# Kernel optimization log

Hardware: AMD Instinct MI355X
Metric: run time of the kernel (lower is better)

The kernel has to match this reference:

```python
import jax, jax.numpy as jnp
import numpy as np

H_SIZE = 2048
NUM_K_HEADS = 16
NUM_V_HEADS = 32
DK = 128
DV = 128
KEY_DIM = NUM_K_HEADS * DK        # 2048
VALUE_DIM = NUM_V_HEADS * DV      # 4096
CONV_DIM = 2 * KEY_DIM + VALUE_DIM  # 8192
KERNEL = 4
EPS = 1e-6
B, S = 2, 2048


def setup_inputs() -> dict:
    key = jax.random.key(0)
    ks = jax.random.split(key, 8)
    w = lambda k, shape, s: jax.random.normal(k, shape, jnp.float32) * s
    return {
        "hidden_states": jax.random.normal(ks[0], (B, S, H_SIZE), jnp.float32),
        "w_qkv": w(ks[1], (H_SIZE, CONV_DIM), 0.02),
        "w_z": w(ks[2], (H_SIZE, VALUE_DIM), 0.02),
        "w_b": w(ks[3], (H_SIZE, NUM_V_HEADS), 0.02),
        "w_a": w(ks[4], (H_SIZE, NUM_V_HEADS), 0.02),
        "conv_w": w(ks[5], (CONV_DIM, KERNEL), 0.2),
        "dt_bias": jnp.ones((NUM_V_HEADS,), jnp.float32),
        "A_log": jnp.zeros((NUM_V_HEADS,), jnp.float32),
        "norm_gamma": jnp.ones((DV,), jnp.float32),
        "w_out": w(ks[6], (VALUE_DIM, H_SIZE), 0.02),
    }


def _l2norm(x, eps=1e-6):
    return x * jax.lax.rsqrt(jnp.sum(x * x, axis=-1, keepdims=True) + eps)


def _causal_conv(x, w):
    # depthwise causal conv1d; x: (B,S,C), w: (C,K)
    K = w.shape[-1]
    Sq = x.shape[1]
    xp = jnp.pad(x, ((0, 0), (K - 1, 0), (0, 0)))
    out = xp[:, 0:Sq, :] * w[None, None, :, 0]
    for j in range(1, K):  # tiny fixed kernel loop (K=4)
        out = out + xp[:, j:j + Sq, :] * w[None, None, :, j]
    return out


def _forward(hidden_states, w_qkv, w_z, w_b, w_a, conv_w, dt_bias, A_log,
             norm_gamma, w_out):
    Bq, Sq, _ = hidden_states.shape
    mixed = hidden_states @ w_qkv                       # (B,S,CONV_DIM)
    z = (hidden_states @ w_z).reshape(Bq, Sq, NUM_V_HEADS, DV)
    b = hidden_states @ w_b                             # (B,S,Hv)
    a = hidden_states @ w_a                             # (B,S,Hv)
    mixed = jax.nn.silu(_causal_conv(mixed, conv_w))
    q, k, v = jnp.split(mixed, [KEY_DIM, 2 * KEY_DIM], axis=-1)
    q = q.reshape(Bq, Sq, NUM_K_HEADS, DK)
    k = k.reshape(Bq, Sq, NUM_K_HEADS, DK)
    v = v.reshape(Bq, Sq, NUM_V_HEADS, DV)
    nrep = NUM_V_HEADS // NUM_K_HEADS
    q = jnp.repeat(q, nrep, axis=2)                     # GQA expand -> Hv heads
    k = jnp.repeat(k, nrep, axis=2)
    beta = jax.nn.sigmoid(b)                            # write gate
    g = -jnp.exp(A_log)[None, None, :] * jax.nn.softplus(a + dt_bias[None, None, :])

    # gated delta rule recurrence in float32 (matches reference)
    qf = _l2norm(q.astype(jnp.float32)) * (DK ** -0.5)
    kf = _l2norm(k.astype(jnp.float32))
    vf = v.astype(jnp.float32)
    gf = g.astype(jnp.float32)
    bf = beta.astype(jnp.float32)

    def step(state, xs):
        q_t, k_t, v_t, g_t, b_t = xs  # (B,H,dk),(B,H,dk),(B,H,dv),(B,H),(B,H)
        state = state * jnp.exp(g_t)[..., None, None]
        kv = jnp.einsum('bhk,bhkv->bhv', k_t, state)
        delta = (v_t - kv) * b_t[..., None]
        state = state + jnp.einsum('bhk,bhv->bhkv', k_t, delta)
        out = jnp.einsum('bhk,bhkv->bhv', q_t, state)
        return state, out

    mv = lambda x: jnp.moveaxis(x, 1, 0)  # (B,S,...) -> (S,B,...)
    xs = (mv(qf), mv(kf), mv(vf), mv(gf), mv(bf))
    state0 = jnp.zeros((Bq, NUM_V_HEADS, DK, DV), jnp.float32)
    _, outs = jax.lax.scan(step, state0, xs)            # (S,B,H,dv)
    o = jnp.moveaxis(outs, 0, 1)                        # (B,S,H,dv)

    # gated RMSNorm over head_v_dim: gate with silu(z), then rms-normalize
    o = o * jax.nn.silu(z.astype(jnp.float32))
    o = o * jax.lax.rsqrt(jnp.mean(o * o, axis=-1, keepdims=True) + EPS)
    o = o * norm_gamma
    o = o.reshape(Bq, Sq, VALUE_DIM).astype(hidden_states.dtype)
    return o @ w_out


def reference(hidden_states, w_qkv, w_z, w_b, w_a, conv_w, dt_bias, A_log,
              norm_gamma, w_out):
    return _forward(hidden_states, w_qkv, w_z, w_b, w_a, conv_w, dt_bias,
                    A_log, norm_gamma, w_out)
```

## Files before the change

### kernel.cpp

```cpp
#include <hip/hip_runtime.h>
#include <hip/hip_bf16.h>
#include <cstdint>


#define HSZ 2048
#define NUM_K_HEADS 16
#define NUM_V_HEADS 32
#define DKH 128
#define DVH 128
#define KEY_DIM 2048
#define VALUE_DIM 4096
#define CONV_DIM 8192
#define BB 2
#define SSEQ 2048
#define MM (BB * SSEQ)
#define CHUNK 64
#define NCHUNK (SSEQ / CHUNK)
#define DVB 16

typedef __hip_bfloat16 bf16;
typedef short short8 __attribute__((ext_vector_type(8)));
typedef float f32x4 __attribute__((ext_vector_type(4)));

__device__ __forceinline__ float bfu(ushort u) {
  union { float f; uint32_t i; } x;
  x.i = ((uint32_t)u) << 16;
  return x.f;
}
__device__ __forceinline__ ushort f2b(float f) {
  bf16 h = __float2bfloat16(f);
  return *reinterpret_cast<ushort*>(&h);
}

__device__ __forceinline__ void gload16(const void* g, const void* l) {
  __builtin_amdgcn_global_load_lds(
      (const __attribute__((address_space(1))) unsigned int*)g,
      (__attribute__((address_space(3))) unsigned int*)(const_cast<void*>(l)),
      16, 0, 0);
}

__device__ __forceinline__ int kidx(int r, int d) {
  return r * 128 + (((d >> 3) ^ (r & 7)) << 3) + (d & 7);
}
__device__ __forceinline__ int widx(int r, int d) {
  return r * 64 + (((d >> 3) ^ (r & 7)) << 3) + (d & 7);
}

__global__ __launch_bounds__(256) void cast_bf16_kernel(
    const float* __restrict__ in, ushort* __restrict__ out, int n4) {
  int i = blockIdx.x * 256 + threadIdx.x;
  if (i < n4) {
    float4 v = ((const float4*)in)[i];
    ushort4 u;
    u.x = f2b(v.x); u.y = f2b(v.y); u.z = f2b(v.z); u.w = f2b(v.w);
    ((ushort4*)out)[i] = u;
  }
}

__global__ __launch_bounds__(256) void transpose_cast(
    const float* __restrict__ W, ushort* __restrict__ WT, int K, int N) {
  __shared__ ushort tile[32][33];
  const int tx = threadIdx.x & 31, ty = threadIdx.x >> 5;
  const int n0 = blockIdx.x * 32, k0 = blockIdx.y * 32;
#pragma unroll
  for (int i = 0; i < 4; ++i)
    tile[ty + i * 8][tx] = f2b(W[(size_t)(k0 + ty + i * 8) * N + n0 + tx]);
  __syncthreads();
#pragma unroll
  for (int i = 0; i < 4; ++i)
    WT[(size_t)(n0 + ty + i * 8) * K + k0 + tx] = tile[tx][ty + i * 8];
}

__global__ __launch_bounds__(512) void gemm256(
    const ushort* __restrict__ A, const ushort* __restrict__ BT,
    ushort* __restrict__ Cv, int M, int N, int K) {
  __shared__ __align__(16) ushort smem[256 * 264];
  const int t = threadIdx.x;
  const int w = t >> 6, lane = t & 63;
  const int m0 = blockIdx.y * 256, n0 = blockIdx.x * 256;
  const int wm = (w >> 2) * 128, wn = (w & 3) * 64;
  const int fr = lane & 15, kb = lane >> 4;
  const int srow = t >> 3;
  const int scol = (t & 7) * 8;
  const int ssw = ((scol >> 3) ^ (srow & 7)) << 3;
  const int rsw = fr & 7;
  f32x4 acc[8][4] = {};
  const int nt = K / 64;

#define STAGE_TILE(tt, buf)                                                   \
  {                                                                           \
    const int k0_ = (tt)*64;                                                  \
    ushort* As_ = smem + (buf)*32768;                                         \
    ushort* Bs_ = As_ + 16384;                                                \
    _Pragma("unroll") for (int p = 0; p < 4; ++p) {                           \
      const int row_ = p * 64 + srow;                                         \
      gload16(&A[(size_t)(m0 + row_) * K + k0_ + ssw],                        \
              &As_[row_ * 64 + scol]);                                        \
    }                                                                         \
    _Pragma("unroll") for (int p = 0; p < 4; ++p) {                           \
      const int row_ = p * 64 + srow;                                         \
      gload16(&BT[(size_t)(n0 + row_) * K + k0_ + ssw],                       \
              &Bs_[row_ * 64 + scol]);                                        \
    }                                                                         \
  }

  STAGE_TILE(0, 0);
  STAGE_TILE(1, 1);

  for (int tt = 0; tt < nt; ++tt) {
    const int buf = tt & 1;
    const ushort* As = smem + buf * 32768;
    const ushort* Bs = As + 16384;
    if (tt + 1 < nt)
      asm volatile("s_waitcnt vmcnt(8)" ::: "memory");
    else
      asm volatile("s_waitcnt vmcnt(0)" ::: "memory");
    __builtin_amdgcn_sched_barrier(0);
    __builtin_amdgcn_s_barrier();
    __builtin_amdgcn_sched_barrier(0);
#pragma unroll
    for (int ks = 0; ks < 2; ++ks) {
      const int kg = ks * 4 + kb;
      const int ca = ((kg ^ rsw) << 3);
      short8 af[8], bf_[4];
#pragma unroll
      for (int mf = 0; mf < 8; ++mf)
        af[mf] = *(const short8*)&As[(wm + mf * 16 + fr) * 64 + ca];
#pragma unroll
      for (int nf = 0; nf < 4; ++nf)
        bf_[nf] = *(const short8*)&Bs[(wn + nf * 16 + fr) * 64 + ca];
#pragma unroll
      for (int mf = 0; mf < 8; ++mf)
#pragma unroll
        for (int nf = 0; nf < 4; ++nf)
          acc[mf][nf] = __builtin_amdgcn_mfma_f32_16x16x32_bf16(
              af[mf], bf_[nf], acc[mf][nf], 0, 0, 0);
    }
    __builtin_amdgcn_sched_barrier(0);
    __builtin_amdgcn_s_barrier();
    __builtin_amdgcn_sched_barrier(0);
    if (tt + 2 < nt) STAGE_TILE(tt + 2, buf);
  }
#undef STAGE_TILE

  const int crow = wm + (lane >> 4) * 4;
  const int ccol = wn + fr;
#pragma unroll
  for (int mf = 0; mf < 8; ++mf)
#pragma unroll
    for (int nf = 0; nf < 4; ++nf)
#pragma unroll
      for (int j = 0; j < 4; ++j)
        smem[(crow + mf * 16 + j) * 264 + ccol + nf * 16] = f2b(acc[mf][nf][j]);
  __syncthreads();
#pragma unroll
  for (int p = 0; p < 16; ++p) {
    const int r = p * 16 + (t >> 5), cch = (t & 31) * 8;
    *(short8*)&Cv[(size_t)(m0 + r) * N + n0 + cch] =
        *(const short8*)&smem[r * 264 + cch];
  }
}

__global__ __launch_bounds__(256) void gemm_mfma_f32(
    const ushort* __restrict__ A, const ushort* __restrict__ BT,
    float* __restrict__ C, int M, int N, int K) {
  __shared__ ushort As[128 * 64];
  __shared__ ushort Bs[128 * 64];
  const int t = threadIdx.x;
  const int w = t >> 6, lane = t & 63;
  const int m0 = blockIdx.y * 128, n0 = blockIdx.x * 128;
  const int srow = lane >> 3;
  const int scol = (lane & 7) * 8;
  const int wm = (w >> 1) * 64, wn = (w & 1) * 64;
  const int fr = lane & 15, kb = lane >> 4;
  f32x4 acc[4][4] = {};

  for (int k0 = 0; k0 < K; k0 += 64) {
#pragma unroll
    for (int i = 0; i < 4; ++i) {
      const int row = (i * 4 + w) * 8 + srow;
      gload16(&A[(size_t)(m0 + row) * K + k0 + scol], &As[row * 64 + scol]);
      gload16(&BT[(size_t)(n0 + row) * K + k0 + scol], &Bs[row * 64 + scol]);
    }
    __syncthreads();
#pragma unroll
    for (int ks = 0; ks < 2; ++ks) {
      const int ka = ks * 32 + kb * 8;
      short8 af[4], bfr[4];
#pragma unroll
      for (int mf = 0; mf < 4; ++mf)
        af[mf] = *(const short8*)&As[(wm + mf * 16 + fr) * 64 + ka];
#pragma unroll
      for (int nf = 0; nf < 4; ++nf)
        bfr[nf] = *(const short8*)&Bs[(wn + nf * 16 + fr) * 64 + ka];
#pragma unroll
      for (int mf = 0; mf < 4; ++mf)
#pragma unroll
        for (int nf = 0; nf < 4; ++nf)
          acc[mf][nf] = __builtin_amdgcn_mfma_f32_16x16x32_bf16(
              af[mf], bfr[nf], acc[mf][nf], 0, 0, 0);
    }
    __syncthreads();
  }
  const int orow = m0 + wm + (lane >> 4) * 4;
  const int ocol = n0 + wn + fr;
#pragma unroll
  for (int mf = 0; mf < 4; ++mf)
#pragma unroll
    for (int nf = 0; nf < 4; ++nf)
#pragma unroll
      for (int j = 0; j < 4; ++j)
        C[(size_t)(orow + mf * 16 + j) * N + ocol + nf * 16] = acc[mf][nf][j];
}

__global__ __launch_bounds__(256) void ba_kernel(
    const float* __restrict__ hs, const float* __restrict__ w_b,
    const float* __restrict__ w_a, const float* __restrict__ dt_bias,
    const float* __restrict__ A_log, float* __restrict__ gbuf,
    float* __restrict__ beta) {
  const int row0 = blockIdx.x * 8;
  const int t = threadIdx.x;
  __shared__ float hsr[8][HSZ];
  __shared__ float red[2][256];
  {
    const float4* src = (const float4*)(hs + (size_t)row0 * HSZ);
    for (int i = t; i < 8 * HSZ / 4; i += 256) ((float4*)hsr)[i] = src[i];
  }
  __syncthreads();
  const int h = t & 31, p = t >> 5;
  float sb[8] = {}, sa[8] = {};
  const int kbeg = p * 256;
  for (int k = kbeg; k < kbeg + 256; ++k) {
    float wb = w_b[k * NUM_V_HEADS + h];
    float wa = w_a[k * NUM_V_HEADS + h];
#pragma unroll
    for (int r = 0; r < 8; ++r) {
      float x = hsr[r][k];
      sb[r] += x * wb;
      sa[r] += x * wa;
    }
  }
#pragma unroll
  for (int r = 0; r < 8; ++r) {
    red[0][t] = sb[r];
    red[1][t] = sa[r];
    __syncthreads();
    if (t < NUM_V_HEADS) {
      float b = 0.f, a = 0.f;
#pragma unroll
      for (int q = 0; q < 8; ++q) {
        b += red[0][t + 32 * q];
        a += red[1][t + 32 * q];
      }
      float bet = 1.f / (1.f + expf(-b));
      float x = a + dt_bias[t];
      float sp = (x > 20.f) ? x : log1pf(expf(x));
      gbuf[(size_t)(row0 + r) * NUM_V_HEADS + t] = -expf(A_log[t]) * sp;
      beta[(size_t)(row0 + r) * NUM_V_HEADS + t] = bet;
    }
    __syncthreads();
  }
}

__global__ __launch_bounds__(256) void conv_kernel(
    const ushort* __restrict__ mixed, const float* __restrict__ conv_w,
    ushort* __restrict__ qkv) {
  const int bid = blockIdx.x;
  const int slice = bid & 3;
  const int row0 = (bid >> 2) * 8;
  const int s0 = row0 & (SSEQ - 1);
  const int t = threadIdx.x;
  const int cbase = slice * 2048 + t * 8;

  float wreg[4][8];
#pragma unroll
  for (int e = 0; e < 8; ++e) {
    float4 wv = *(const float4*)&conv_w[(cbase + e) * 4];
    wreg[0][e] = wv.x;
    wreg[1][e] = wv.y;
    wreg[2][e] = wv.z;
    wreg[3][e] = wv.w;
  }

  const ushort* mp = mixed + (size_t)row0 * CONV_DIM + cbase;
  short8 win[4];
  const short8 z8 = {0, 0, 0, 0, 0, 0, 0, 0};
#pragma unroll
  for (int j = 0; j < 3; ++j)
    win[j] = (s0 - 3 + j >= 0) ? *(const short8*)&mp[(ptrdiff_t)(j - 3) * CONV_DIM]
                               : z8;

  if (slice < 2) {
    float vals[8][8];
    float ssq[8];
#pragma unroll
    for (int r = 0; r < 8; ++r) {
      win[3] = *(const short8*)&mp[(ptrdiff_t)r * CONV_DIM];
      float sq = 0.f;
#pragma unroll
      for (int e = 0; e < 8; ++e) {
        float a = bfu((ushort)win[0][e]) * wreg[0][e] +
                  bfu((ushort)win[1][e]) * wreg[1][e] +
                  bfu((ushort)win[2][e]) * wreg[2][e] +
                  bfu((ushort)win[3][e]) * wreg[3][e];
        float x = a / (1.f + expf(-a));
        vals[r][e] = x;
        sq += x * x;
      }
      ssq[r] = sq;
      win[0] = win[1];
      win[1] = win[2];
      win[2] = win[3];
    }
#pragma unroll
    for (int r = 0; r < 8; ++r) {
      float sq = ssq[r];
      sq += __shfl_xor(sq, 1, 64);
      sq += __shfl_xor(sq, 2, 64);
      sq += __shfl_xor(sq, 4, 64);
      sq += __shfl_xor(sq, 8, 64);
      float sc = rsqrtf(sq + 1e-6f);
      if (slice == 0) sc *= 0.08838834764831845f;
      short8 o;
#pragma unroll
      for (int e = 0; e < 8; ++e) o[e] = (short)f2b(vals[r][e] * sc);
      *(short8*)&qkv[(size_t)(row0 + r) * CONV_DIM + cbase] = o;
    }
  } else {
#pragma unroll
    for (int r = 0; r < 8; ++r) {
      win[3] = *(const short8*)&mp[(ptrdiff_t)r * CONV_DIM];
      short8 o;
#pragma unroll
      for (int e = 0; e < 8; ++e) {
        float a = bfu((ushort)win[0][e]) * wreg[0][e] +
                  bfu((ushort)win[1][e]) * wreg[1][e] +
                  bfu((ushort)win[2][e]) * wreg[2][e] +
                  bfu((ushort)win[3][e]) * wreg[3][e];
        o[e] = (short)f2b(a / (1.f + expf(-a)));
      }
      *(short8*)&qkv[(size_t)(row0 + r) * CONV_DIM + cbase] = o;
      win[0] = win[1];
      win[1] = win[2];
      win[2] = win[3];
    }
  }
}

__global__ __launch_bounds__(256) void chunk_T_kernel(
    const ushort* __restrict__ qkv, const float* __restrict__ gbuf,
    const float* __restrict__ beta, ushort* __restrict__ Tbuf,
    ushort* __restrict__ Wbuf) {
  const int bid = blockIdx.x;
  const int c = bid & 31;
  const int h = (bid >> 5) & 31;
  const int b = bid >> 10;
  const int hk = h >> 1;
  const int t = threadIdx.x;
  const int w = t >> 6, lane = t & 63;
  const int fr = lane & 15, fq = lane >> 4;

  __shared__ ushort Klds[64 * 128];
  __shared__ ushort Qlds[64 * 128];
  __shared__ __align__(16) float AT[64][68];
  __shared__ ushort Wlds[64 * 64];
  __shared__ float Gs[64], Bsh[64];

  const int row0 = b * SSEQ + c * CHUNK;
  const int qcol = hk * DKH;
  const int kcol = KEY_DIM + hk * DKH;

#pragma unroll
  for (int r = 0; r < 4; ++r) {
    int vi = t + 256 * r;
    int row = vi >> 4, gr = vi & 15;
    const size_t gb = (size_t)(row0 + row) * CONV_DIM;
    *(short8*)&Klds[row * 128 + ((gr ^ (row & 7)) << 3)] =
        *(const short8*)&qkv[gb + kcol + gr * 8];
    *(short8*)&Qlds[row * 128 + ((gr ^ (row & 7)) << 3)] =
        *(const short8*)&qkv[gb + qcol + gr * 8];
  }
  if (t < 64) {
    float s = gbuf[(size_t)(row0 + t) * NUM_V_HEADS + h];
#pragma unroll
    for (int off = 1; off < 64; off <<= 1) {
      float p = __shfl_up(s, off, 64);
      if (lane >= off) s += p;
    }
    Gs[t] = s;
    Bsh[t] = beta[(size_t)(row0 + t) * NUM_V_HEADS + h];
  }
  __syncthreads();

  f32x4 kkt[4] = {}, qkt[4] = {};
#pragma unroll
  for (int ks = 0; ks < 4; ++ks) {
    int d0 = ks * 32 + fq * 8;
    short8 xk = *(const short8*)&Klds[kidx(w * 16 + fr, d0)];
    short8 xq = *(const short8*)&Qlds[kidx(w * 16 + fr, d0)];
#pragma unroll
    for (int j = 0; j < 4; ++j) {
      short8 yk = *(const short8*)&Klds[kidx(j * 16 + fr, d0)];
      kkt[j] = __builtin_amdgcn_mfma_f32_16x16x32_bf16(xk, yk, kkt[j], 0, 0, 0);
      qkt[j] = __builtin_amdgcn_mfma_f32_16x16x32_bf16(xq, yk, qkt[j], 0, 0, 0);
    }
  }
#pragma unroll
  for (int j = 0; j < 4; ++j)
#pragma unroll
    for (int jj = 0; jj < 4; ++jj) {
      int i = w * 16 + fq * 4 + jj;
      int jc = j * 16 + fr;
      AT[jc][i] = (jc < i) ? Bsh[i] * __expf(Gs[i] - Gs[jc]) * kkt[j][jj] : 0.f;
      float val = (jc <= i) ? __expf(Gs[i] - Gs[jc]) * qkt[j][jj] : 0.f;
      Wlds[widx(i, jc)] = f2b(val);
    }
  __syncthreads();

  {
    ushort* Wg = Wbuf + (size_t)bid * 4096;
#pragma unroll
    for (int e = 0; e < 8; ++e)
      ((uint*)Wg)[e * 256 + t] = ((const uint*)Wlds)[e * 256 + t];
  }

  if (w == 0) {
    float u[64];
#pragma unroll
    for (int i = 0; i < 64; ++i) u[i] = (i == lane) ? 1.f : 0.f;
#pragma unroll
    for (int j = 0; j < 63; ++j) {
      float xj = u[j];
      const int i0 = (j + 1) & ~3;
#pragma unroll
      for (int ii = i0; ii < 64; ii += 4) {
        float4 a4 = *(const float4*)&AT[j][ii];
        if (ii + 0 > j) u[ii + 0] -= a4.x * xj;
        if (ii + 1 > j) u[ii + 1] -= a4.y * xj;
        if (ii + 2 > j) u[ii + 2] -= a4.z * xj;
        if (ii + 3 > j) u[ii + 3] -= a4.w * xj;
      }
    }
    ushort* Tg = Tbuf + (size_t)bid * 4096;
#pragma unroll
    for (int i = 0; i < 64; ++i) Tg[i * 64 + lane] = f2b(u[i]);
  }
}

__global__ __launch_bounds__(256, 2) void recur_chunk_kernel(
    const ushort* __restrict__ qkv, const float* __restrict__ gbuf,
    const float* __restrict__ beta, const ushort* __restrict__ Tbuf,
    const ushort* __restrict__ Wbuf, float* __restrict__ o) {
  const int bid = blockIdx.x;
  const int dvq = bid & 7;
  const int h = (bid >> 3) & 31;
  const int b = bid >> 8;
  const int hk = h >> 1;
  const int t = threadIdx.x;
  const int w = t >> 6, lane = t & 63;
  const int fr = lane & 15, fq = lane >> 4;

  __shared__ ushort Klds[64 * 128];
  __shared__ ushort Vlds[64 * DVB];
  __shared__ ushort Sth[DVB * 128];
  __shared__ ushort Stl[DVB * 128];
  __shared__ ushort Th[64 * 64];
  __shared__ ushort Wlds[64 * 64];
  __shared__ ushort Ut[DVB * 64];
  __shared__ ushort UTs[DVB * 64];
  __shared__ ushort UTo[DVB * 64];
  __shared__ float Gs[64], Bsh[64];

  float sreg[2][4] = {};

  const int qcol = hk * DKH;
  const int kcol = KEY_DIM + hk * DKH;
  const int vcol = 2 * KEY_DIM + h * DVH + dvq * DVB;
  const int ocol = h * DVH + dvq * DVB;
  const size_t tbase0 = ((size_t)(b * 32 + h) * 32) * 4096;

  for (int c = 0; c < NCHUNK; ++c) {
    const int row0 = b * SSEQ + c * CHUNK;

    short8 xq[4];
#pragma unroll
    for (int ks = 0; ks < 4; ++ks)
      xq[ks] = *(const short8*)&qkv[(size_t)(row0 + w * 16 + fr) * CONV_DIM +
                                    qcol + ks * 32 + fq * 8];
    const ushort* Tg = Tbuf + tbase0 + (size_t)c * 4096;
    const ushort* Wg = Wbuf + tbase0 + (size_t)c * 4096;
    short8 tv0 = *(const short8*)&Tg[t * 16];
    short8 tv1 = *(const short8*)&Tg[t * 16 + 8];
#pragma unroll
    for (int e = 0; e < 8; ++e)
      ((uint*)Wlds)[e * 256 + t] = ((const uint*)Wg)[e * 256 + t];
#pragma unroll
    for (int r = 0; r < 4; ++r) {
      int vi = t + 256 * r;
      int row = vi >> 4, gr = vi & 15;
      *(short8*)&Klds[row * 128 + ((gr ^ (row & 7)) << 3)] =
          *(const short8*)&qkv[(size_t)(row0 + row) * CONV_DIM + kcol + gr * 8];
    }
    if (t < 128) {
      int row = t >> 1, c0 = (t & 1) * 8;
      *(short8*)&Vlds[row * DVB + c0] =
          *(const short8*)&qkv[(size_t)(row0 + row) * CONV_DIM + vcol + c0];
    }
    if (t < 64) {
      float s = gbuf[(size_t)(row0 + t) * NUM_V_HEADS + h];
#pragma unroll
      for (int off = 1; off < 64; off <<= 1) {
        float p = __shfl_up(s, off, 64);
        if (lane >= off) s += p;
      }
      Gs[t] = s;
      Bsh[t] = beta[(size_t)(row0 + t) * NUM_V_HEADS + h];
    }
#pragma unroll
    for (int dt = 0; dt < 2; ++dt)
#pragma unroll
      for (int jj = 0; jj < 4; ++jj) {
        int d = (w * 2 + dt) * 16 + fq * 4 + jj;
        float f = sreg[dt][jj];
        ushort hi = f2b(f);
        int idx = kidx(fr, d);
        Sth[idx] = hi;
        Stl[idx] = f2b(f - bfu(hi));
      }
    {
      int r = t >> 2, d0 = (t & 3) * 16;
      *(short8*)&Th[widx(r, d0)] = tv0;
      *(short8*)&Th[widx(r, d0 + 8)] = tv1;
    }
    __syncthreads();

    f32x4 ks0 = {}, qs0 = {};
#pragma unroll
    for (int ks = 0; ks < 4; ++ks) {
      int d0 = ks * 32 + fq * 8;
      short8 xk = *(const short8*)&Klds[kidx(w * 16 + fr, d0)];
      short8 yh = *(const short8*)&Sth[kidx(fr, d0)];
      short8 yl = *(const short8*)&Stl[kidx(fr, d0)];
      ks0 = __builtin_amdgcn_mfma_f32_16x16x32_bf16(xk, yh, ks0, 0, 0, 0);
      ks0 = __builtin_amdgcn_mfma_f32_16x16x32_bf16(xk, yl, ks0, 0, 0, 0);
      qs0 = __builtin_amdgcn_mfma_f32_16x16x32_bf16(xq[ks], yh, qs0, 0, 0, 0);
      qs0 = __builtin_amdgcn_mfma_f32_16x16x32_bf16(xq[ks], yl, qs0, 0, 0, 0);
    }
    f32x4 oacc;
#pragma unroll
    for (int jj = 0; jj < 4; ++jj) {
      int i = w * 16 + fq * 4 + jj;
      float eg = __expf(Gs[i]);
      float rhs = Bsh[i] * (bfu(Vlds[i * DVB + fr]) - eg * ks0[jj]);
      Ut[widx(fr, i)] = f2b(rhs);
      oacc[jj] = qs0[jj] * eg;
    }
    __syncthreads();

    {
      f32x4 uacc = {};
#pragma unroll
      for (int ks = 0; ks < 2; ++ks) {
        int j0 = ks * 32 + fq * 8;
        short8 ta = *(const short8*)&Th[widx(w * 16 + fr, j0)];
        short8 ub = *(const short8*)&Ut[widx(fr, j0)];
        uacc = __builtin_amdgcn_mfma_f32_16x16x32_bf16(ta, ub, uacc, 0, 0, 0);
      }
#pragma unroll
      for (int jj = 0; jj < 4; ++jj) {
        int i = w * 16 + fq * 4 + jj;
        float u = uacc[jj];
        UTo[widx(fr, i)] = f2b(u);
        UTs[widx(fr, i)] = f2b(u * __expf(Gs[63] - Gs[i]));
      }
    }
    __syncthreads();

#pragma unroll
    for (int ks = 0; ks < 2; ++ks) {
      int i0 = ks * 32 + fq * 8;
      short8 xw = *(const short8*)&Wlds[widx(w * 16 + fr, i0)];
      short8 yu = *(const short8*)&UTo[widx(fr, i0)];
      oacc = __builtin_amdgcn_mfma_f32_16x16x32_bf16(xw, yu, oacc, 0, 0, 0);
    }
#pragma unroll
    for (int jj = 0; jj < 4; ++jj) {
      int tt = w * 16 + fq * 4 + jj;
      o[(size_t)(row0 + tt) * VALUE_DIM + ocol + fr] = oacc[jj];
    }
    {
      float eGC = __expf(Gs[63]);
#pragma unroll
      for (int dt = 0; dt < 2; ++dt) {
        const int dk0 = (w * 2 + dt) * 16;
        f32x4 sacc;
#pragma unroll
        for (int jj = 0; jj < 4; ++jj) sacc[jj] = sreg[dt][jj] * eGC;
        const int dkr = dk0 + fr;
#pragma unroll
        for (int ks = 0; ks < 2; ++ks) {
          short8 xk;
#pragma unroll
          for (int e = 0; e < 8; ++e)
            xk[e] = (short)Klds[kidx(ks * 32 + fq * 8 + e, dkr)];
          short8 yu = *(const short8*)&UTs[widx(fr, ks * 32 + fq * 8)];
          sacc = __builtin_amdgcn_mfma_f32_16x16x32_bf16(xk, yu, sacc, 0, 0, 0);
        }
#pragma unroll
        for (int jj = 0; jj < 4; ++jj) sreg[dt][jj] = sacc[jj];
      }
    }
    __syncthreads();
  }
}

__global__ __launch_bounds__(256) void gnorm_kernel(
    const float* __restrict__ o, const ushort* __restrict__ z,
    const float* __restrict__ gamma, ushort* __restrict__ ob) {
  const int row = blockIdx.x;
  const int t = threadIdx.x;
  const int grp = t >> 3, r = t & 7;
  const float* op = o + (size_t)row * VALUE_DIM + grp * DVH + r * 16;
  const ushort* zp = z + (size_t)row * VALUE_DIM + grp * DVH + r * 16;
  ushort* obp = ob + (size_t)row * VALUE_DIM + grp * DVH + r * 16;
  float vals[16];
  float ssq = 0.f;
#pragma unroll
  for (int i = 0; i < 16; ++i) {
    float zz = bfu(zp[i]);
    float x = op[i] * (zz / (1.f + expf(-zz)));
    vals[i] = x;
    ssq += x * x;
  }
  ssq += __shfl_xor(ssq, 1, 64);
  ssq += __shfl_xor(ssq, 2, 64);
  ssq += __shfl_xor(ssq, 4, 64);
  float sc = rsqrtf(ssq * (1.f / 128.f) + 1e-6f);
#pragma unroll
  for (int i = 0; i < 16; ++i) obp[i] = f2b(vals[i] * sc * gamma[r * 16 + i]);
}

extern "C" void kernel_launch(void* const* d_in, const int* in_sizes, int n_in,
                              void* d_out, int out_size, void* d_ws,
                              size_t ws_size, hipStream_t stream) {
  const float* hs = (const float*)d_in[0];
  const float* w_qkv = (const float*)d_in[1];
  const float* w_z = (const float*)d_in[2];
  const float* w_b = (const float*)d_in[3];
  const float* w_a = (const float*)d_in[4];
  const float* conv_w = (const float*)d_in[5];
  const float* dt_bias = (const float*)d_in[6];
  const float* A_log = (const float*)d_in[7];
  const float* gamma = (const float*)d_in[8];
  const float* w_out = (const float*)d_in[9];
  float* out = (float*)d_out;
  char* wsb = (char*)d_ws;

  ushort* hs_b = (ushort*)wsb;
  ushort* wqkvT = hs_b + (size_t)MM * HSZ;
  ushort* wzT = wqkvT + (size_t)CONV_DIM * HSZ;
  ushort* woutT = wzT + (size_t)VALUE_DIM * HSZ;
  ushort* mixed = woutT + (size_t)HSZ * VALUE_DIM;
  ushort* qkv = mixed + (size_t)MM * CONV_DIM;
  ushort* z = qkv + (size_t)MM * CONV_DIM;
  float* gbuf = (float*)(z + (size_t)MM * VALUE_DIM);
  float* beta = gbuf + (size_t)MM * NUM_V_HEADS;
  float* o = (float*)mixed;
  ushort* ob = qkv;
  ushort* Tbuf = hs_b;
  ushort* Wbuf = wqkvT;

  cast_bf16_kernel<<<(MM * HSZ / 4 + 255) / 256, 256, 0, stream>>>(
      hs, hs_b, MM * HSZ / 4);
  transpose_cast<<<dim3(CONV_DIM / 32, HSZ / 32), 256, 0, stream>>>(
      w_qkv, wqkvT, HSZ, CONV_DIM);
  transpose_cast<<<dim3(VALUE_DIM / 32, HSZ / 32), 256, 0, stream>>>(
      w_z, wzT, HSZ, VALUE_DIM);
  transpose_cast<<<dim3(HSZ / 32, VALUE_DIM / 32), 256, 0, stream>>>(
      w_out, woutT, VALUE_DIM, HSZ);

  gemm256<<<dim3(CONV_DIM / 256, MM / 256), 512, 0, stream>>>(
      hs_b, wqkvT, mixed, MM, CONV_DIM, HSZ);
  gemm256<<<dim3(VALUE_DIM / 256, MM / 256), 512, 0, stream>>>(
      hs_b, wzT, z, MM, VALUE_DIM, HSZ);
  ba_kernel<<<MM / 8, 256, 0, stream>>>(hs, w_b, w_a, dt_bias, A_log, gbuf,
                                        beta);
  conv_kernel<<<2048, 256, 0, stream>>>(mixed, conv_w, qkv);
  chunk_T_kernel<<<2048, 256, 0, stream>>>(qkv, gbuf, beta, Tbuf, Wbuf);
  recur_chunk_kernel<<<512, 256, 0, stream>>>(qkv, gbuf, beta, Tbuf, Wbuf, o);
  gnorm_kernel<<<MM, 256, 0, stream>>>(o, z, gamma, ob);
  gemm_mfma_f32<<<dim3(HSZ / 128, MM / 128), 256, 0, stream>>>(
      ob, woutT, out, MM, HSZ, VALUE_DIM);
}
```

Measured before the change: 729.6 us.

## Double-buffer output GEMM with swizzled LDS and vectorize gated norm

The output projection GEMM now double-buffers its LDS tiles, prefetching two k-steps ahead with explicit vmcnt waits and raw s_barrier calls so global loads overlap with MFMA work. It also applies an XOR swizzle to LDS columns to reduce bank conflicts, and sets launch bounds to allow two blocks per CU. Separately, the gated RMSNorm kernel now uses vectorized float4 and short8 loads and stores. The cost is doubled LDS use per block and more delicate synchronization that depends on exact vmcnt counting.

New measurement: 695.1 us. 1.05x faster.

```diff
diff --git a/kernel.cpp b/kernel.cpp
--- a/kernel.cpp
+++ b/kernel.cpp
@@ -161,38 +161,64 @@
   }
 }
 
-__global__ __launch_bounds__(256) void gemm_mfma_f32(
+__global__ __launch_bounds__(256, 2) void gemm128_f32(
     const ushort* __restrict__ A, const ushort* __restrict__ BT,
     float* __restrict__ C, int M, int N, int K) {
-  __shared__ ushort As[128 * 64];
-  __shared__ ushort Bs[128 * 64];
+  __shared__ __align__(16) ushort smem[2 * 16384];
   const int t = threadIdx.x;
   const int w = t >> 6, lane = t & 63;
   const int m0 = blockIdx.y * 128, n0 = blockIdx.x * 128;
-  const int srow = lane >> 3;
-  const int scol = (lane & 7) * 8;
   const int wm = (w >> 1) * 64, wn = (w & 1) * 64;
   const int fr = lane & 15, kb = lane >> 4;
+  const int srow = t >> 3;
+  const int scol = (t & 7) * 8;
+  const int ssw = ((scol >> 3) ^ (srow & 7)) << 3;
+  const int rsw = fr & 7;
   f32x4 acc[4][4] = {};
-
-  for (int k0 = 0; k0 < K; k0 += 64) {
-#pragma unroll
-    for (int i = 0; i < 4; ++i) {
-      const int row = (i * 4 + w) * 8 + srow;
-      gload16(&A[(size_t)(m0 + row) * K + k0 + scol], &As[row * 64 + scol]);
-      gload16(&BT[(size_t)(n0 + row) * K + k0 + scol], &Bs[row * 64 + scol]);
-    }
-    __syncthreads();
+  const int nt = K / 64;
+
+#define STAGE128(tt, buf)                                                     \
+  {                                                                           \
+    const int k0_ = (tt)*64;                                                  \
+    ushort* As_ = smem + (buf)*16384;                                         \
+    ushort* Bs_ = As_ + 8192;                                                 \
+    _Pragma("unroll") for (int p = 0; p < 4; ++p) {                           \
+      const int row_ = p * 32 + srow;                                         \
+      gload16(&A[(size_t)(m0 + row_) * K + k0_ + ssw],                        \
+              &As_[row_ * 64 + scol]);                                        \
+    }                                                                         \
+    _Pragma("unroll") for (int p = 0; p < 4; ++p) {                           \
+      const int row_ = p * 32 + srow;                                         \
+      gload16(&BT[(size_t)(n0 + row_) * K + k0_ + ssw],                       \
+              &Bs_[row_ * 64 + scol]);                                        \
+    }                                                                         \
+  }
+
+  STAGE128(0, 0);
+  STAGE128(1, 1);
+
+  for (int tt = 0; tt < nt; ++tt) {
+    const int buf = tt & 1;
+    const ushort* As = smem + buf * 16384;
+    const ushort* Bs = As + 8192;
+    if (tt + 1 < nt)
+      asm volatile("s_waitcnt vmcnt(8)" ::: "memory");
+    else
+      asm volatile("s_waitcnt vmcnt(0)" ::: "memory");
+    __builtin_amdgcn_sched_barrier(0);
+    __builtin_amdgcn_s_barrier();
+    __builtin_amdgcn_sched_barrier(0);
 #pragma unroll
     for (int ks = 0; ks < 2; ++ks) {
-      const int ka = ks * 32 + kb * 8;
+      const int kg = ks * 4 + kb;
+      const int ca = ((kg ^ rsw) << 3);
       short8 af[4], bfr[4];
 #pragma unroll
       for (int mf = 0; mf < 4; ++mf)
-        af[mf] = *(const short8*)&As[(wm + mf * 16 + fr) * 64 + ka];
+        af[mf] = *(const short8*)&As[(wm + mf * 16 + fr) * 64 + ca];
 #pragma unroll
       for (int nf = 0; nf < 4; ++nf)
-        bfr[nf] = *(const short8*)&Bs[(wn + nf * 16 + fr) * 64 + ka];
+        bfr[nf] = *(const short8*)&Bs[(wn + nf * 16 + fr) * 64 + ca];
 #pragma unroll
       for (int mf = 0; mf < 4; ++mf)
 #pragma unroll
@@ -200,8 +226,13 @@
           acc[mf][nf] = __builtin_amdgcn_mfma_f32_16x16x32_bf16(
               af[mf], bfr[nf], acc[mf][nf], 0, 0, 0);
     }
-    __syncthreads();
-  }
+    __builtin_amdgcn_sched_barrier(0);
+    __builtin_amdgcn_s_barrier();
+    __builtin_amdgcn_sched_barrier(0);
+    if (tt + 2 < nt) STAGE128(tt + 2, buf);
+  }
+#undef STAGE128
+
   const int orow = m0 + wm + (lane >> 4) * 4;
   const int ocol = n0 + wn + fr;
 #pragma unroll
@@ -623,12 +654,19 @@
   const float* op = o + (size_t)row * VALUE_DIM + grp * DVH + r * 16;
   const ushort* zp = z + (size_t)row * VALUE_DIM + grp * DVH + r * 16;
   ushort* obp = ob + (size_t)row * VALUE_DIM + grp * DVH + r * 16;
+  float4 ov[4];
+  short8 zv[2];
+#pragma unroll
+  for (int q = 0; q < 4; ++q) ov[q] = *(const float4*)&op[q * 4];
+  zv[0] = *(const short8*)&zp[0];
+  zv[1] = *(const short8*)&zp[8];
   float vals[16];
   float ssq = 0.f;
 #pragma unroll
   for (int i = 0; i < 16; ++i) {
-    float zz = bfu(zp[i]);
-    float x = op[i] * (zz / (1.f + expf(-zz)));
+    float zz = bfu((ushort)zv[i >> 3][i & 7]);
+    float oo = ((const float*)&ov[i >> 2])[i & 3];
+    float x = oo * (zz / (1.f + expf(-zz)));
     vals[i] = x;
     ssq += x * x;
   }
@@ -636,8 +674,14 @@
   ssq += __shfl_xor(ssq, 2, 64);
   ssq += __shfl_xor(ssq, 4, 64);
   float sc = rsqrtf(ssq * (1.f / 128.f) + 1e-6f);
-#pragma unroll
-  for (int i = 0; i < 16; ++i) obp[i] = f2b(vals[i] * sc * gamma[r * 16 + i]);
+  short8 o0, o1;
+#pragma unroll
+  for (int i = 0; i < 8; ++i) {
+    o0[i] = (short)f2b(vals[i] * sc * gamma[r * 16 + i]);
+    o1[i] = (short)f2b(vals[8 + i] * sc * gamma[r * 16 + 8 + i]);
+  }
+  *(short8*)&obp[0] = o0;
+  *(short8*)&obp[8] = o1;
 }
 
 extern "C" void kernel_launch(void* const* d_in, const int* in_sizes, int n_in,
@@ -689,6 +733,6 @@
   chunk_T_kernel<<<2048, 256, 0, stream>>>(qkv, gbuf, beta, Tbuf, Wbuf);
   recur_chunk_kernel<<<512, 256, 0, stream>>>(qkv, gbuf, beta, Tbuf, Wbuf, o);
   gnorm_kernel<<<MM, 256, 0, stream>>>(o, z, gamma, ob);
-  gemm_mfma_f32<<<dim3(HSZ / 128, MM / 128), 256, 0, stream>>>(
+  gemm128_f32<<<dim3(HSZ / 128, MM / 128), 256, 0, stream>>>(
       ob, woutT, out, MM, HSZ, VALUE_DIM);
 }
```
